# Performance work log

Hardware: AMD Instinct MI355X
Metric: run time of the kernel (lower is better)

The kernel has to match this reference:

```python
import jax, jax.numpy as jnp
import numpy as np

R = 16
ALPHA = 32.0
SCALING = ALPHA / max(1, R)

def setup_inputs() -> dict:
    key = jax.random.key(0)
    ks = jax.random.split(key, 7)
    B_, D, M = 16384, 1024, 4096
    return {
        "x": jax.random.normal(ks[0], (B_, D), dtype=jnp.float32),
        "W0": jax.random.normal(ks[1], (M, D), dtype=jnp.float32) * 0.02,
        "b0": jax.random.normal(ks[2], (M,), dtype=jnp.float32) * 0.02,
        "A": jax.random.normal(ks[3], (R, D), dtype=jnp.float32) * 0.001,
        "B": jax.random.normal(ks[4], (M, R), dtype=jnp.float32) * 0.02,
        "W2": jax.random.normal(ks[5], (1, M), dtype=jnp.float32) * 0.02,
        "b2": jax.random.normal(ks[6], (1,), dtype=jnp.float32) * 0.02,
    }

def reference(x, W0, b0, A, B, W2, b2):
    # effective_W = W0 + scaling * (B @ A)  -> [m_hidden, d_in]
    W_eff = W0 + SCALING * (B @ A)
    # F.linear(x, W_eff, b0): x @ W_eff^T + b0 -> [batch, m_hidden]
    h = jax.nn.relu(jnp.einsum('bd,md->bm', x, W_eff) + b0)
    # fc2: [batch, 1] then squeeze(-1)
    out = (jnp.einsum('bm,om->bo', h, W2) + b2).squeeze(-1)
    return out
```

## Files before the change

kernel.cpp:

```cpp
#include <hip/hip_runtime.h>
#include <hip/hip_bf16.h>
#include <stdint.h>

#define BATCH  16384
#define D_IN   1024
#define M_HID  4096
#define R_LORA 16
#define SCALING 2.0f

#define STRIP    64
#define NTHREADS 512

typedef __bf16 bf16x8 __attribute__((ext_vector_type(8)));
typedef float  f32x16 __attribute__((ext_vector_type(16)));

__device__ __forceinline__ unsigned short f2bf(float f) {
    union { float f; unsigned int u; } c; c.f = f;
    unsigned int u = c.u;
    return (unsigned short)((u + 0x7FFFu + ((u >> 16) & 1u)) >> 16);
}

__global__ __launch_bounds__(256) void k_wprep(
    const float* __restrict__ W0, const float* __restrict__ A,
    const float* __restrict__ Bl, unsigned short* __restrict__ wb)
{
    int id = blockIdx.x * 256 + threadIdx.x;
    int rl  = id & 31;
    int c   = (id >> 5) & 127;
    int n32 = id >> 12;
    int n = n32 * 32 + rl, k0 = c * 8;
    const float* wr = W0 + (size_t)n * D_IN + k0;
    float4 v0 = *(const float4*)(wr);
    float4 v1 = *(const float4*)(wr + 4);
    const float* brow = Bl + n * R_LORA;
#pragma unroll
    for (int r = 0; r < R_LORA; ++r) {
        float s = SCALING * brow[r];
        const float* ar = A + r * D_IN + k0;
        float4 a0 = *(const float4*)(ar);
        float4 a1 = *(const float4*)(ar + 4);
        v0.x += s * a0.x; v0.y += s * a0.y; v0.z += s * a0.z; v0.w += s * a0.w;
        v1.x += s * a1.x; v1.y += s * a1.y; v1.z += s * a1.z; v1.w += s * a1.w;
    }
    uint4 o;
    o.x = (unsigned)f2bf(v0.x) | ((unsigned)f2bf(v0.y) << 16);
    o.y = (unsigned)f2bf(v0.z) | ((unsigned)f2bf(v0.w) << 16);
    o.z = (unsigned)f2bf(v1.x) | ((unsigned)f2bf(v1.y) << 16);
    o.w = (unsigned)f2bf(v1.z) | ((unsigned)f2bf(v1.w) << 16);
    ((uint4*)wb)[id] = o;
}

__global__ __launch_bounds__(NTHREADS, 2) void k_strip(
    const float* __restrict__ xf, const unsigned short* __restrict__ wb,
    const float* __restrict__ b0, const float* __restrict__ W2,
    const float* __restrict__ b2, float* __restrict__ out)
{
    __shared__ unsigned short As[STRIP * D_IN];
    __shared__ float red[8][STRIP];

    const int tid  = threadIdx.x;
    const int lane = tid & 63;
    const int wave = tid >> 6;
    const int rl   = lane & 31;
    const int half = lane >> 5;
    const int row0 = blockIdx.x * STRIP;

    {
        const int r  = tid >> 3;
        const int c0 = tid & 7;
        const float* xr = xf + (size_t)(row0 + r) * D_IN;
#pragma unroll
        for (int i = 0; i < 16; ++i) {
            int c = i * 8 + c0;
            float4 v0 = *(const float4*)(xr + c * 8);
            float4 v1 = *(const float4*)(xr + c * 8 + 4);
            uint4 o;
            o.x = (unsigned)f2bf(v0.x) | ((unsigned)f2bf(v0.y) << 16);
            o.y = (unsigned)f2bf(v0.z) | ((unsigned)f2bf(v0.w) << 16);
            o.z = (unsigned)f2bf(v1.x) | ((unsigned)f2bf(v1.y) << 16);
            o.w = (unsigned)f2bf(v1.z) | ((unsigned)f2bf(v1.w) << 16);
            *(uint4*)(&As[c * 512 + r * 8]) = o;
        }
    }
    __syncthreads();

    float rowpart[2][16];
#pragma unroll
    for (int ti = 0; ti < 2; ++ti)
#pragma unroll
        for (int r = 0; r < 16; ++r) rowpart[ti][r] = 0.f;

    for (int pass = 0; pass < 8; ++pass) {
        const int n0 = wave * 64 + pass * 512;
        const float w2a = W2[n0 + rl],      b0a = b0[n0 + rl];
        const float w2b = W2[n0 + 32 + rl], b0b = b0[n0 + 32 + rl];
        const int n32 = wave * 2 + pass * 16;
        const unsigned short* w0p = wb + (size_t)n32 * 32768 + half * 256 + rl * 8;
        const unsigned short* w1p = w0p + 32768;

        f32x16 acc[2][2] = {};
        bf16x8 wf0[4], wf1[4];
#pragma unroll
        for (int p = 0; p < 4; ++p) {
            wf0[p] = *(const bf16x8*)(w0p + p * 512);
            wf1[p] = *(const bf16x8*)(w1p + p * 512);
        }

#pragma unroll 4
        for (int kk = 0; kk < 64; ++kk) {
            const int cur = kk & 3;
            const int coff = (kk * 2 + half) * 512 + rl * 8;
            bf16x8 af0 = *(const bf16x8*)(&As[coff]);
            bf16x8 af1 = *(const bf16x8*)(&As[coff + 256]);
            bf16x8 w0c = wf0[cur], w1c = wf1[cur];
            if (kk < 60) {
                wf0[cur] = *(const bf16x8*)(w0p + (kk + 4) * 512);
                wf1[cur] = *(const bf16x8*)(w1p + (kk + 4) * 512);
            }
            acc[0][0] = __builtin_amdgcn_mfma_f32_32x32x16_bf16(af0, w0c, acc[0][0], 0, 0, 0);
            acc[0][1] = __builtin_amdgcn_mfma_f32_32x32x16_bf16(af0, w1c, acc[0][1], 0, 0, 0);
            acc[1][0] = __builtin_amdgcn_mfma_f32_32x32x16_bf16(af1, w0c, acc[1][0], 0, 0, 0);
            acc[1][1] = __builtin_amdgcn_mfma_f32_32x32x16_bf16(af1, w1c, acc[1][1], 0, 0, 0);
        }

#pragma unroll
        for (int ti = 0; ti < 2; ++ti)
#pragma unroll
            for (int r = 0; r < 16; ++r)
                rowpart[ti][r] += fmaxf(acc[ti][0][r] + b0a, 0.f) * w2a
                                + fmaxf(acc[ti][1][r] + b0b, 0.f) * w2b;
    }

#pragma unroll
    for (int ti = 0; ti < 2; ++ti)
#pragma unroll
        for (int r = 0; r < 16; ++r) {
            float p = rowpart[ti][r];
#pragma unroll
            for (int m = 1; m <= 16; m <<= 1)
                p += __shfl_xor(p, m, 64);
            if (rl == 0)
                red[wave][ti * 32 + (r & 3) + 8 * (r >> 2) + 4 * half] = p;
        }
    __syncthreads();
    if (tid < STRIP) {
        float s = b2[0];
#pragma unroll
        for (int w = 0; w < 8; ++w) s += red[w][tid];
        out[row0 + tid] = s;
    }
}

__global__ __launch_bounds__(256) void k_naive(
    const float* __restrict__ x, const float* __restrict__ W0,
    const float* __restrict__ b0, const float* __restrict__ A,
    const float* __restrict__ Bl, const float* __restrict__ W2,
    const float* __restrict__ b2, float* __restrict__ out)
{
    __shared__ float xs[D_IN];
    int b = blockIdx.x;
    for (int d = threadIdx.x; d < D_IN; d += 256) xs[d] = x[(size_t)b * D_IN + d];
    __syncthreads();
    float part = 0.f;
    for (int m = threadIdx.x; m < M_HID; m += 256) {
        float h = b0[m];
        const float* wr = W0 + (size_t)m * D_IN;
        const float* brow = Bl + m * R_LORA;
        for (int d = 0; d < D_IN; ++d) {
            float w = wr[d];
            for (int r = 0; r < R_LORA; ++r) w += SCALING * brow[r] * A[r * D_IN + d];
            h += xs[d] * w;
        }
        part += fmaxf(h, 0.f) * W2[m];
    }
    __shared__ float sred[256];
    sred[threadIdx.x] = part;
    __syncthreads();
    for (int s = 128; s > 0; s >>= 1) {
        if (threadIdx.x < s) sred[threadIdx.x] += sred[threadIdx.x + s];
        __syncthreads();
    }
    if (threadIdx.x == 0) out[b] = sred[0] + b2[0];
}

extern "C" void kernel_launch(void* const* d_in, const int* in_sizes, int n_in,
                              void* d_out, int out_size, void* d_ws, size_t ws_size,
                              hipStream_t stream) {
    const float* x  = (const float*)d_in[0];
    const float* W0 = (const float*)d_in[1];
    const float* b0 = (const float*)d_in[2];
    const float* A  = (const float*)d_in[3];
    const float* Bl = (const float*)d_in[4];
    const float* W2 = (const float*)d_in[5];
    const float* b2 = (const float*)d_in[6];
    float* out = (float*)d_out;

    const size_t wb_bytes = (size_t)M_HID * D_IN * 2;
    if (ws_size >= wb_bytes) {
        unsigned short* wb = (unsigned short*)d_ws;
        hipLaunchKernelGGL(k_wprep, dim3(M_HID * D_IN / 8 / 256), dim3(256), 0, stream,
                           W0, A, Bl, wb);
        hipLaunchKernelGGL(k_strip, dim3(BATCH / STRIP), dim3(NTHREADS), 0, stream,
                           x, wb, b0, W2, b2, out);
    } else {
        hipLaunchKernelGGL(k_naive, dim3(BATCH), dim3(256), 0, stream,
                           x, W0, b0, A, Bl, W2, b2, out);
    }
}
```

Measured before the change: 250.3 us.

## Use 128-row strips split over hidden halves with double-buffered x staging

Adds a new main kernel that works on 128-row batch strips, with each block covering half of the hidden dimension, so 256 blocks are launched. x is converted to bf16 in K-chunks of 256 into a double-buffered, XOR-swizzled LDS tile, overlapping the global loads with MFMA work. Each W fragment is now reused across four 32-row tiles, and the bias/ReLU/W2 epilogue reduces into LDS after each pass. A small reduce kernel adds the two hidden-half partials and b2. This adds a third launch and workspace for the partials, in exchange for halving weight traffic per row.

```diff
diff --git a/kernel.cpp b/kernel.cpp
--- a/kernel.cpp
+++ b/kernel.cpp
@@ -8,25 +8,26 @@
 #define R_LORA 16
 #define SCALING 2.0f
 
+
 #define STRIP    64
 #define NTHREADS 512
 
 typedef __bf16 bf16x8 __attribute__((ext_vector_type(8)));
 typedef float  f32x16 __attribute__((ext_vector_type(16)));
 
-__device__ __forceinline__ unsigned short f2bf(float f) {
-    union { float f; unsigned int u; } c; c.f = f;
-    unsigned int u = c.u;
-    return (unsigned short)((u + 0x7FFFu + ((u >> 16) & 1u)) >> 16);
+__device__ __forceinline__ unsigned f2bf(float f) {
+    union { float f; unsigned u; } c; c.f = f;
+    unsigned u = c.u;
+    return ((u + 0x7FFFu + ((u >> 16) & 1u)) >> 16);
 }
 
 __global__ __launch_bounds__(256) void k_wprep(
     const float* __restrict__ W0, const float* __restrict__ A,
     const float* __restrict__ Bl, unsigned short* __restrict__ wb)
 {
-    int id = blockIdx.x * 256 + threadIdx.x;
-    int rl  = id & 31;
-    int c   = (id >> 5) & 127;
+    int id  = blockIdx.x * 256 + threadIdx.x;
+    int c   = id & 127;
+    int rl  = (id >> 7) & 31;
     int n32 = id >> 12;
     int n = n32 * 32 + rl, k0 = c * 8;
     const float* wr = W0 + (size_t)n * D_IN + k0;
@@ -43,11 +44,170 @@
         v1.x += s * a1.x; v1.y += s * a1.y; v1.z += s * a1.z; v1.w += s * a1.w;
     }
     uint4 o;
-    o.x = (unsigned)f2bf(v0.x) | ((unsigned)f2bf(v0.y) << 16);
-    o.y = (unsigned)f2bf(v0.z) | ((unsigned)f2bf(v0.w) << 16);
-    o.z = (unsigned)f2bf(v1.x) | ((unsigned)f2bf(v1.y) << 16);
-    o.w = (unsigned)f2bf(v1.z) | ((unsigned)f2bf(v1.w) << 16);
-    ((uint4*)wb)[id] = o;
+    o.x = f2bf(v0.x) | (f2bf(v0.y) << 16);
+    o.y = f2bf(v0.z) | (f2bf(v0.w) << 16);
+    o.z = f2bf(v1.x) | (f2bf(v1.y) << 16);
+    o.w = f2bf(v1.z) | (f2bf(v1.w) << 16);
+    *(uint4*)(&wb[(size_t)n32 * 32768 + c * 256 + rl * 8]) = o;
+}
+
+__global__ __launch_bounds__(512, 2) void k_strip128(
+    const float* __restrict__ xf, const unsigned short* __restrict__ wb,
+    const float* __restrict__ b0, const float* __restrict__ W2,
+    float* __restrict__ part)
+{
+    __shared__ unsigned short As[2 * 32768];
+    __shared__ float redacc[8][128];
+
+    const int tid  = threadIdx.x;
+    const int lane = tid & 63;
+    const int wave = tid >> 6;
+    const int rl   = lane & 31;
+    const int half = lane >> 5;
+
+    const int b     = blockIdx.x;
+    const int mhalf = (b >> 2) & 1;
+    const int strip = (b & 3) * 32 + (b >> 3);
+    const int row0  = strip * 128;
+
+    ((float*)redacc)[tid]       = 0.f;
+    ((float*)redacc)[tid + 512] = 0.f;
+
+    const int so  = tid & 31;
+    const int sr0 = tid >> 5;
+
+    {
+        const float* xsrc = xf + (size_t)row0 * D_IN + so * 8;
+        uint4 st[8];
+#pragma unroll
+        for (int j = 0; j < 8; ++j) {
+            const float* p = xsrc + (size_t)(sr0 + j * 16) * D_IN;
+            float4 v0 = *(const float4*)(p);
+            float4 v1 = *(const float4*)(p + 4);
+            st[j].x = f2bf(v0.x) | (f2bf(v0.y) << 16);
+            st[j].y = f2bf(v0.z) | (f2bf(v0.w) << 16);
+            st[j].z = f2bf(v1.x) | (f2bf(v1.y) << 16);
+            st[j].w = f2bf(v1.z) | (f2bf(v1.w) << 16);
+        }
+#pragma unroll
+        for (int j = 0; j < 8; ++j) {
+            int row = sr0 + j * 16;
+            int cs  = so ^ (row & 31);
+            *(uint4*)(&As[row * 256 + cs * 8]) = st[j];
+        }
+    }
+    __syncthreads();
+
+    f32x16 acc[4][2];
+    bf16x8 wf0[2], wf1[2];
+    const unsigned short* w0p = wb;
+    const unsigned short* w1p = wb;
+    float b0a = 0.f, b0b = 0.f, w2a = 0.f, w2b = 0.f;
+
+    for (int e = 0; e < 16; ++e) {
+        const int pass = e >> 2, kc = e & 3, cb = e & 1;
+
+        if (kc == 0) {
+            const int n0  = mhalf * 2048 + pass * 512 + wave * 64;
+            const int n32 = n0 >> 5;
+            w0p = wb + (size_t)n32 * 32768 + half * 256 + rl * 8;
+            w1p = w0p + 32768;
+            b0a = b0[n0 + rl];      b0b = b0[n0 + 32 + rl];
+            w2a = W2[n0 + rl];      w2b = W2[n0 + 32 + rl];
+#pragma unroll
+            for (int ti = 0; ti < 4; ++ti)
+#pragma unroll
+                for (int cj = 0; cj < 2; ++cj)
+#pragma unroll
+                    for (int r = 0; r < 16; ++r) acc[ti][cj][r] = 0.f;
+#pragma unroll
+            for (int p2 = 0; p2 < 2; ++p2) {
+                wf0[p2] = *(const bf16x8*)(w0p + p2 * 512);
+                wf1[p2] = *(const bf16x8*)(w1p + p2 * 512);
+            }
+        }
+
+        uint4 st[8];
+        const bool do_stage = (e < 15);
+        if (do_stage) {
+            const int nkc = (e + 1) & 3;
+            const float* xsrc = xf + (size_t)row0 * D_IN + nkc * 256 + so * 8;
+#pragma unroll
+            for (int j = 0; j < 8; ++j) {
+                const float* p = xsrc + (size_t)(sr0 + j * 16) * D_IN;
+                float4 v0 = *(const float4*)(p);
+                float4 v1 = *(const float4*)(p + 4);
+                st[j].x = f2bf(v0.x) | (f2bf(v0.y) << 16);
+                st[j].y = f2bf(v0.z) | (f2bf(v0.w) << 16);
+                st[j].z = f2bf(v1.x) | (f2bf(v1.y) << 16);
+                st[j].w = f2bf(v1.z) | (f2bf(v1.w) << 16);
+            }
+        }
+
+        const unsigned short* Ab = As + cb * 32768;
+#pragma unroll 4
+        for (int kk = 0; kk < 16; ++kk) {
+            const int kkg = kc * 16 + kk;
+            const int cur = kkg & 1;
+            const int oc  = kk * 2 + half;
+            bf16x8 af[4];
+#pragma unroll
+            for (int ti = 0; ti < 4; ++ti) {
+                const int row = ti * 32 + rl;
+                af[ti] = *(const bf16x8*)(Ab + row * 256 + ((oc ^ rl) << 3));
+            }
+            bf16x8 w0c = wf0[cur], w1c = wf1[cur];
+            if (kkg < 62) {
+                wf0[cur] = *(const bf16x8*)(w0p + (kkg + 2) * 512);
+                wf1[cur] = *(const bf16x8*)(w1p + (kkg + 2) * 512);
+            }
+#pragma unroll
+            for (int ti = 0; ti < 4; ++ti) {
+                acc[ti][0] = __builtin_amdgcn_mfma_f32_32x32x16_bf16(af[ti], w0c, acc[ti][0], 0, 0, 0);
+                acc[ti][1] = __builtin_amdgcn_mfma_f32_32x32x16_bf16(af[ti], w1c, acc[ti][1], 0, 0, 0);
+            }
+        }
+
+        if (kc == 3) {
+#pragma unroll
+            for (int ti = 0; ti < 4; ++ti)
+#pragma unroll
+                for (int r = 0; r < 16; ++r) {
+                    float p = fmaxf(acc[ti][0][r] + b0a, 0.f) * w2a
+                            + fmaxf(acc[ti][1][r] + b0b, 0.f) * w2b;
+#pragma unroll
+                    for (int m = 1; m <= 16; m <<= 1)
+                        p += __shfl_xor(p, m, 64);
+                    if (rl == 0)
+                        redacc[wave][ti * 32 + (r & 3) + 8 * (r >> 2) + 4 * half] += p;
+                }
+        }
+
+        if (do_stage) {
+#pragma unroll
+            for (int j = 0; j < 8; ++j) {
+                int row = sr0 + j * 16;
+                int cs  = so ^ (row & 31);
+                *(uint4*)(&As[(cb ^ 1) * 32768 + row * 256 + cs * 8]) = st[j];
+            }
+        }
+        __syncthreads();
+    }
+
+    if (tid < 128) {
+        float s = 0.f;
+#pragma unroll
+        for (int w = 0; w < 8; ++w) s += redacc[w][tid];
+        part[(size_t)mhalf * BATCH + row0 + tid] = s;
+    }
+}
+
+__global__ __launch_bounds__(256) void k_reduce(
+    const float* __restrict__ part, const float* __restrict__ b2,
+    float* __restrict__ out)
+{
+    int i = blockIdx.x * 256 + threadIdx.x;
+    out[i] = part[i] + part[BATCH + i] + b2[0];
 }
 
 __global__ __launch_bounds__(NTHREADS, 2) void k_strip(
@@ -75,10 +235,10 @@
             float4 v0 = *(const float4*)(xr + c * 8);
             float4 v1 = *(const float4*)(xr + c * 8 + 4);
             uint4 o;
-            o.x = (unsigned)f2bf(v0.x) | ((unsigned)f2bf(v0.y) << 16);
-            o.y = (unsigned)f2bf(v0.z) | ((unsigned)f2bf(v0.w) << 16);
-            o.z = (unsigned)f2bf(v1.x) | ((unsigned)f2bf(v1.y) << 16);
-            o.w = (unsigned)f2bf(v1.z) | ((unsigned)f2bf(v1.w) << 16);
+            o.x = f2bf(v0.x) | (f2bf(v0.y) << 16);
+            o.y = f2bf(v0.z) | (f2bf(v0.w) << 16);
+            o.z = f2bf(v1.x) | (f2bf(v1.y) << 16);
+            o.w = f2bf(v1.z) | (f2bf(v1.w) << 16);
             *(uint4*)(&As[c * 512 + r * 8]) = o;
         }
     }
@@ -195,8 +355,19 @@
     const float* b2 = (const float*)d_in[6];
     float* out = (float*)d_out;
 
-    const size_t wb_bytes = (size_t)M_HID * D_IN * 2;
-    if (ws_size >= wb_bytes) {
+    const size_t wb_bytes   = (size_t)M_HID * D_IN * 2;
+    const size_t part_bytes = (size_t)2 * BATCH * sizeof(float);
+
+    if (ws_size >= wb_bytes + part_bytes) {
+        unsigned short* wb = (unsigned short*)d_ws;
+        float* part = (float*)((char*)d_ws + wb_bytes);
+        hipLaunchKernelGGL(k_wprep, dim3(M_HID * D_IN / 8 / 256), dim3(256), 0, stream,
+                           W0, A, Bl, wb);
+        hipLaunchKernelGGL(k_strip128, dim3(256), dim3(512), 0, stream,
+                           x, wb, b0, W2, part);
+        hipLaunchKernelGGL(k_reduce, dim3(BATCH / 256), dim3(256), 0, stream,
+                           part, b2, out);
+    } else if (ws_size >= wb_bytes) {
         unsigned short* wb = (unsigned short*)d_ws;
         hipLaunchKernelGGL(k_wprep, dim3(M_HID * D_IN / 8 / 256), dim3(256), 0, stream,
                            W0, A, Bl, wb);
```

Result: slower. 309.1 us (+23.5%).

## Double waves per strip block, swizzle LDS layout, reduce per pass

Applied to the files above, without the earlier changes.

Raises the strip kernel to 1024 threads (16 waves) covering the hidden dimension in 4 passes instead of 8, aiming for more latency hiding per CU given one LDS-bound block per CU. The activation tile in LDS is rewritten as row-major with an XOR swizzle to keep fragment reads conflict-free. Per-row partial sums are now reduced and accumulated into shared memory each pass, freeing the register-held rowpart array. The weight-prep kernel also loads the LoRA B row with vector loads, and the prefetch loop is peeled to drop a branch. The launch bound of (1024,4) may force a tight register budget and cause spills.

```diff
diff --git a/kernel.cpp b/kernel.cpp
--- a/kernel.cpp
+++ b/kernel.cpp
@@ -8,16 +8,14 @@
 #define R_LORA 16
 #define SCALING 2.0f
 
-#define STRIP    64
-#define NTHREADS 512
 
 typedef __bf16 bf16x8 __attribute__((ext_vector_type(8)));
 typedef float  f32x16 __attribute__((ext_vector_type(16)));
 
-__device__ __forceinline__ unsigned short f2bf(float f) {
-    union { float f; unsigned int u; } c; c.f = f;
-    unsigned int u = c.u;
-    return (unsigned short)((u + 0x7FFFu + ((u >> 16) & 1u)) >> 16);
+__device__ __forceinline__ unsigned f2bf(float f) {
+    union { float f; unsigned u; } c; c.f = f;
+    unsigned u = c.u;
+    return ((u + 0x7FFFu + ((u >> 16) & 1u)) >> 16);
 }
 
 __global__ __launch_bounds__(256) void k_wprep(
@@ -33,9 +31,18 @@
     float4 v0 = *(const float4*)(wr);
     float4 v1 = *(const float4*)(wr + 4);
     const float* brow = Bl + n * R_LORA;
+    float4 bb[4];
+    bb[0] = *(const float4*)(brow);
+    bb[1] = *(const float4*)(brow + 4);
+    bb[2] = *(const float4*)(brow + 8);
+    bb[3] = *(const float4*)(brow + 12);
+    const float bs[16] = { bb[0].x, bb[0].y, bb[0].z, bb[0].w,
+                           bb[1].x, bb[1].y, bb[1].z, bb[1].w,
+                           bb[2].x, bb[2].y, bb[2].z, bb[2].w,
+                           bb[3].x, bb[3].y, bb[3].z, bb[3].w };
 #pragma unroll
     for (int r = 0; r < R_LORA; ++r) {
-        float s = SCALING * brow[r];
+        float s = SCALING * bs[r];
         const float* ar = A + r * D_IN + k0;
         float4 a0 = *(const float4*)(ar);
         float4 a1 = *(const float4*)(ar + 4);
@@ -43,58 +50,55 @@
         v1.x += s * a1.x; v1.y += s * a1.y; v1.z += s * a1.z; v1.w += s * a1.w;
     }
     uint4 o;
-    o.x = (unsigned)f2bf(v0.x) | ((unsigned)f2bf(v0.y) << 16);
-    o.y = (unsigned)f2bf(v0.z) | ((unsigned)f2bf(v0.w) << 16);
-    o.z = (unsigned)f2bf(v1.x) | ((unsigned)f2bf(v1.y) << 16);
-    o.w = (unsigned)f2bf(v1.z) | ((unsigned)f2bf(v1.w) << 16);
+    o.x = f2bf(v0.x) | (f2bf(v0.y) << 16);
+    o.y = f2bf(v0.z) | (f2bf(v0.w) << 16);
+    o.z = f2bf(v1.x) | (f2bf(v1.y) << 16);
+    o.w = f2bf(v1.z) | (f2bf(v1.w) << 16);
     ((uint4*)wb)[id] = o;
 }
 
-__global__ __launch_bounds__(NTHREADS, 2) void k_strip(
+__global__ __launch_bounds__(1024, 4) void k_strip(
     const float* __restrict__ xf, const unsigned short* __restrict__ wb,
     const float* __restrict__ b0, const float* __restrict__ W2,
     const float* __restrict__ b2, float* __restrict__ out)
 {
-    __shared__ unsigned short As[STRIP * D_IN];
-    __shared__ float red[8][STRIP];
+    __shared__ unsigned short As[64 * 1024];
+    __shared__ float red[16][64];
 
     const int tid  = threadIdx.x;
     const int lane = tid & 63;
     const int wave = tid >> 6;
     const int rl   = lane & 31;
     const int half = lane >> 5;
-    const int row0 = blockIdx.x * STRIP;
+    const int row0 = blockIdx.x * 64;
+
+    ((float*)red)[tid] = 0.f;
 
     {
-        const int r  = tid >> 3;
-        const int c0 = tid & 7;
-        const float* xr = xf + (size_t)(row0 + r) * D_IN;
-#pragma unroll
-        for (int i = 0; i < 16; ++i) {
-            int c = i * 8 + c0;
-            float4 v0 = *(const float4*)(xr + c * 8);
-            float4 v1 = *(const float4*)(xr + c * 8 + 4);
+        const int so8 = tid & 127;
+        const int rb  = tid >> 7;
+        const float* xsrc = xf + (size_t)row0 * D_IN + so8 * 8;
+#pragma unroll
+        for (int j = 0; j < 8; ++j) {
+            const int r = j * 8 + rb;
+            const float* p = xsrc + (size_t)r * D_IN;
+            float4 v0 = *(const float4*)(p);
+            float4 v1 = *(const float4*)(p + 4);
             uint4 o;
-            o.x = (unsigned)f2bf(v0.x) | ((unsigned)f2bf(v0.y) << 16);
-            o.y = (unsigned)f2bf(v0.z) | ((unsigned)f2bf(v0.w) << 16);
-            o.z = (unsigned)f2bf(v1.x) | ((unsigned)f2bf(v1.y) << 16);
-            o.w = (unsigned)f2bf(v1.z) | ((unsigned)f2bf(v1.w) << 16);
-            *(uint4*)(&As[c * 512 + r * 8]) = o;
-        }
-    }
-    __syncthreads();
-
-    float rowpart[2][16];
-#pragma unroll
-    for (int ti = 0; ti < 2; ++ti)
-#pragma unroll
-        for (int r = 0; r < 16; ++r) rowpart[ti][r] = 0.f;
-
-    for (int pass = 0; pass < 8; ++pass) {
-        const int n0 = wave * 64 + pass * 512;
+            o.x = f2bf(v0.x) | (f2bf(v0.y) << 16);
+            o.y = f2bf(v0.z) | (f2bf(v0.w) << 16);
+            o.z = f2bf(v1.x) | (f2bf(v1.y) << 16);
+            o.w = f2bf(v1.z) | (f2bf(v1.w) << 16);
+            *(uint4*)(&As[r * 1024 + ((so8 ^ (r & 31)) << 3)]) = o;
+        }
+    }
+    __syncthreads();
+
+    for (int pass = 0; pass < 4; ++pass) {
+        const int n0 = pass * 1024 + wave * 64;
         const float w2a = W2[n0 + rl],      b0a = b0[n0 + rl];
         const float w2b = W2[n0 + 32 + rl], b0b = b0[n0 + 32 + rl];
-        const int n32 = wave * 2 + pass * 16;
+        const int n32 = n0 >> 5;
         const unsigned short* w0p = wb + (size_t)n32 * 32768 + half * 256 + rl * 8;
         const unsigned short* w1p = w0p + 32768;
 
@@ -107,46 +111,50 @@
         }
 
 #pragma unroll 4
-        for (int kk = 0; kk < 64; ++kk) {
+        for (int kk = 0; kk < 60; ++kk) {
             const int cur = kk & 3;
-            const int coff = (kk * 2 + half) * 512 + rl * 8;
-            bf16x8 af0 = *(const bf16x8*)(&As[coff]);
-            bf16x8 af1 = *(const bf16x8*)(&As[coff + 256]);
+            const int oc  = kk * 2 + half;
+            bf16x8 af0 = *(const bf16x8*)(&As[rl * 1024 + ((oc ^ rl) << 3)]);
+            bf16x8 af1 = *(const bf16x8*)(&As[(32 + rl) * 1024 + ((oc ^ rl) << 3)]);
             bf16x8 w0c = wf0[cur], w1c = wf1[cur];
-            if (kk < 60) {
-                wf0[cur] = *(const bf16x8*)(w0p + (kk + 4) * 512);
-                wf1[cur] = *(const bf16x8*)(w1p + (kk + 4) * 512);
-            }
+            wf0[cur] = *(const bf16x8*)(w0p + (kk + 4) * 512);
+            wf1[cur] = *(const bf16x8*)(w1p + (kk + 4) * 512);
             acc[0][0] = __builtin_amdgcn_mfma_f32_32x32x16_bf16(af0, w0c, acc[0][0], 0, 0, 0);
             acc[0][1] = __builtin_amdgcn_mfma_f32_32x32x16_bf16(af0, w1c, acc[0][1], 0, 0, 0);
             acc[1][0] = __builtin_amdgcn_mfma_f32_32x32x16_bf16(af1, w0c, acc[1][0], 0, 0, 0);
             acc[1][1] = __builtin_amdgcn_mfma_f32_32x32x16_bf16(af1, w1c, acc[1][1], 0, 0, 0);
         }
+#pragma unroll
+        for (int kk = 60; kk < 64; ++kk) {
+            const int cur = kk & 3;
+            const int oc  = kk * 2 + half;
+            bf16x8 af0 = *(const bf16x8*)(&As[rl * 1024 + ((oc ^ rl) << 3)]);
+            bf16x8 af1 = *(const bf16x8*)(&As[(32 + rl) * 1024 + ((oc ^ rl) << 3)]);
+            acc[0][0] = __builtin_amdgcn_mfma_f32_32x32x16_bf16(af0, wf0[cur], acc[0][0], 0, 0, 0);
+            acc[0][1] = __builtin_amdgcn_mfma_f32_32x32x16_bf16(af0, wf1[cur], acc[0][1], 0, 0, 0);
+            acc[1][0] = __builtin_amdgcn_mfma_f32_32x32x16_bf16(af1, wf0[cur], acc[1][0], 0, 0, 0);
+            acc[1][1] = __builtin_amdgcn_mfma_f32_32x32x16_bf16(af1, wf1[cur], acc[1][1], 0, 0, 0);
+        }
 
 #pragma unroll
         for (int ti = 0; ti < 2; ++ti)
 #pragma unroll
-            for (int r = 0; r < 16; ++r)
-                rowpart[ti][r] += fmaxf(acc[ti][0][r] + b0a, 0.f) * w2a
-                                + fmaxf(acc[ti][1][r] + b0b, 0.f) * w2b;
-    }
-
-#pragma unroll
-    for (int ti = 0; ti < 2; ++ti)
-#pragma unroll
-        for (int r = 0; r < 16; ++r) {
-            float p = rowpart[ti][r];
-#pragma unroll
-            for (int m = 1; m <= 16; m <<= 1)
-                p += __shfl_xor(p, m, 64);
-            if (rl == 0)
-                red[wave][ti * 32 + (r & 3) + 8 * (r >> 2) + 4 * half] = p;
-        }
-    __syncthreads();
-    if (tid < STRIP) {
+            for (int r = 0; r < 16; ++r) {
+                float p = fmaxf(acc[ti][0][r] + b0a, 0.f) * w2a
+                        + fmaxf(acc[ti][1][r] + b0b, 0.f) * w2b;
+#pragma unroll
+                for (int m = 1; m <= 16; m <<= 1)
+                    p += __shfl_xor(p, m, 64);
+                if (rl == 0)
+                    red[wave][ti * 32 + (r & 3) + 8 * (r >> 2) + 4 * half] += p;
+            }
+    }
+
+    __syncthreads();
+    if (tid < 64) {
         float s = b2[0];
 #pragma unroll
-        for (int w = 0; w < 8; ++w) s += red[w][tid];
+        for (int w = 0; w < 16; ++w) s += red[w][tid];
         out[row0 + tid] = s;
     }
 }
@@ -200,7 +208,7 @@
         unsigned short* wb = (unsigned short*)d_ws;
         hipLaunchKernelGGL(k_wprep, dim3(M_HID * D_IN / 8 / 256), dim3(256), 0, stream,
                            W0, A, Bl, wb);
-        hipLaunchKernelGGL(k_strip, dim3(BATCH / STRIP), dim3(NTHREADS), 0, stream,
+        hipLaunchKernelGGL(k_strip, dim3(BATCH / 64), dim3(1024), 0, stream,
                            x, wb, b0, W2, b2, out);
     } else {
         hipLaunchKernelGGL(k_naive, dim3(BATCH), dim3(256), 0, stream,
```

New measurement: 267.1 us. +6.7%, slower.
